# Performance work log

Hardware: AMD Instinct MI355X
Metric: run time of the kernel (lower is better)

Reference implementation:

```python
import jax, jax.numpy as jnp
import numpy as np

S, B, DM, H, DFF = 2048, 4, 1024, 16, 4096
DK = DM // H  # 64, dv == dk
EPS = 1e-5

def layer_norm(x, g, b):
    mu = jnp.mean(x, axis=-1, keepdims=True)
    var = jnp.var(x, axis=-1, keepdims=True)
    return (x - mu) * jax.lax.rsqrt(var + EPS) * g + b

def setup_inputs() -> dict:
    key = jax.random.key(0)
    ks = jax.random.split(key, 12)
    sc = 0.02
    return {
        "X": jax.random.normal(ks[0], (S, B, DM), dtype=jnp.float32),
        # stacked per-head projections: weight [H, dk, dm], bias [H, dk]
        "WQ_w": jax.random.normal(ks[1], (H, DK, DM), dtype=jnp.float32) * sc,
        "WQ_b": jnp.zeros((H, DK), dtype=jnp.float32),
        "WK_w": jax.random.normal(ks[2], (H, DK, DM), dtype=jnp.float32) * sc,
        "WK_b": jnp.zeros((H, DK), dtype=jnp.float32),
        "WV_w": jax.random.normal(ks[3], (H, DK, DM), dtype=jnp.float32) * sc,
        "WV_b": jnp.zeros((H, DK), dtype=jnp.float32),
        "WO_w": jax.random.normal(ks[4], (DM, H * DK), dtype=jnp.float32) * sc,
        "WO_b": jnp.zeros((DM,), dtype=jnp.float32),
        "ln1_g": jnp.ones((DM,), dtype=jnp.float32),
        "ln1_b": jnp.zeros((DM,), dtype=jnp.float32),
        "W1": jax.random.normal(ks[5], (DFF, DM), dtype=jnp.float32) * sc,
        "b1": jnp.zeros((DFF,), dtype=jnp.float32),
        "W2": jax.random.normal(ks[6], (DM, DFF), dtype=jnp.float32) * sc,
        "b2": jnp.zeros((DM,), dtype=jnp.float32),
        "ln2_g": jnp.ones((DM,), dtype=jnp.float32),
        "ln2_b": jnp.zeros((DM,), dtype=jnp.float32),
    }

def reference(X, WQ_w, WQ_b, WK_w, WK_b, WV_w, WV_b, WO_w, WO_b,
              ln1_g, ln1_b, W1, b1, W2, b2, ln2_g, ln2_b):
    # --- self-attention (encoder: no causal mask, no key_mask, drop=0) ---
    # X: [S, B, DM]; per-head Q/K/V: [S, B, H, DK]
    Q = jnp.einsum('sbd,hkd->sbhk', X, WQ_w) + WQ_b
    K = jnp.einsum('sbd,hkd->sbhk', X, WK_w) + WK_b
    V = jnp.einsum('sbd,hvd->sbhv', X, WV_w) + WV_b
    scores = jnp.einsum('sbhk,lbhk->sbhl', Q, K) / jnp.sqrt(jnp.float32(DK))
    attn = jax.nn.softmax(scores, axis=-1)  # softmax over keys l
    ctx = jnp.einsum('sbhl,lbhv->sbhv', attn, V)
    # concat heads (head-major order matches torch.concat over head list)
    ctx = ctx.reshape(S, B, H * DK)
    y = ctx @ WO_w.T + WO_b
    X1 = layer_norm(y + X, ln1_g, ln1_b)
    # --- MLP (1 hidden layer, ReLU) ---
    h = jax.nn.relu(X1 @ W1.T + b1)
    m = h @ W2.T + b2
    return layer_norm(m + X1, ln2_g, ln2_b)
```

## Files before the change

### kernel.cpp

```cpp
#include <hip/hip_runtime.h>
#include <stdint.h>

typedef short bf16x8 __attribute__((ext_vector_type(8)));
typedef float f32x4 __attribute__((ext_vector_type(4)));
typedef float f32x16 __attribute__((ext_vector_type(16)));

__device__ __forceinline__ float bf2f(uint16_t u) {
    union { uint32_t i; float f; } c; c.i = ((uint32_t)u) << 16; return c.f;
}
__device__ __forceinline__ uint16_t f2bf(float f) {
    union { float f; uint32_t i; } c; c.f = f;
    uint32_t x = c.i;
    return (uint16_t)((x + 0x7fffu + ((x >> 16) & 1u)) >> 16);
}
__device__ __forceinline__ uint32_t pack2t(float lo, float hi) {
    union { float f; uint32_t u; } a, b;
    a.f = lo; b.f = hi;
    return __builtin_amdgcn_perm(b.u, a.u, 0x07060302u);
}

__device__ __forceinline__ void load_lds16(const void* g, void* lds) {
    using gp_t = const __attribute__((address_space(1))) uint32_t*;
    using lp_t = __attribute__((address_space(3))) uint32_t*;
    __builtin_amdgcn_global_load_lds(
        reinterpret_cast<gp_t>(reinterpret_cast<uintptr_t>(g)),
        reinterpret_cast<lp_t>((uint32_t)reinterpret_cast<uintptr_t>(lds)),
        16, 0, 0);
}

__global__ __launch_bounds__(256) void cvt_all(
    const float* __restrict__ X,
    const float* __restrict__ wqf, const float* __restrict__ wkf,
    const float* __restrict__ wvf, const float* __restrict__ wof,
    const float* __restrict__ w1f, const float* __restrict__ w2f,
    const float* __restrict__ bqf, const float* __restrict__ bkf,
    const float* __restrict__ bvf, const float* __restrict__ bof,
    const float* __restrict__ b1f, const float* __restrict__ b2f,
    uint16_t* __restrict__ Xb, uint16_t* __restrict__ wd, uint16_t* __restrict__ bd)
{
    const int b = blockIdx.x, tid = threadIdx.x;
    const size_t M = 1048576ull;
    const float* s; uint16_t* d; size_t i, off;
    if (b < 8192) {
        i = ((size_t)b * 256 + tid) * 4;
        s = X; off = i; d = Xb;
    } else if (b < 20480) {
        i = ((size_t)(b - 8192) * 256 + tid) * 4;
        d = wd;
        if (i < M)           { s = wqf; off = i; }
        else if (i < 2 * M)  { s = wkf; off = i - M; }
        else if (i < 3 * M)  { s = wvf; off = i - 2 * M; }
        else if (i < 4 * M)  { s = wof; off = i - 3 * M; }
        else if (i < 8 * M)  { s = w1f; off = i - 4 * M; }
        else                 { s = w2f; off = i - 8 * M; }
    } else {
        int j = tid * 4;
        d = bd;
        for (int p = 0; p < 9; ++p, j += 1024) {
            const float* sb; int ob;
            if (j < 1024)      { sb = bqf; ob = j; }
            else if (j < 2048) { sb = bkf; ob = j - 1024; }
            else if (j < 3072) { sb = bvf; ob = j - 2048; }
            else if (j < 4096) { sb = bof; ob = j - 3072; }
            else if (j < 8192) { sb = b1f; ob = j - 4096; }
            else               { sb = b2f; ob = j - 8192; }
            float4 x = *(const float4*)(sb + ob);
            ushort4 u;
            u.x = f2bf(x.x); u.y = f2bf(x.y); u.z = f2bf(x.z); u.w = f2bf(x.w);
            *(ushort4*)(d + j) = u;
        }
        return;
    }
    float4 x = *(const float4*)(s + off);
    ushort4 u;
    u.x = f2bf(x.x); u.y = f2bf(x.y); u.z = f2bf(x.z); u.w = f2bf(x.w);
    *(ushort4*)(d + i) = u;
}

template<int MODE, int NT>
__global__ __launch_bounds__(256) void gemm_bt(
    const uint16_t* __restrict__ A, const uint16_t* __restrict__ B,
    const uint16_t* __restrict__ bias, uint16_t* __restrict__ C,
    int K, int N, int relu)
{
    const int CT = NT / 32;
    __shared__ uint16_t sA[128 * 64];
    __shared__ uint16_t sB[NT * 64];
    const int tid = threadIdx.x;
    const int w = tid >> 6, ln = tid & 63;
    const int m = ln & 15, q = ln >> 4;
    const int wr = w >> 1, wc = w & 1;
    const int tm = blockIdx.y * 128, tn = blockIdx.x * NT;

    f32x4 zero = {0.f, 0.f, 0.f, 0.f};
    f32x4 acc[4][CT];
#pragma unroll
    for (int i = 0; i < 4; ++i)
#pragma unroll
        for (int j = 0; j < CT; ++j) acc[i][j] = zero;

    const int sr = tid >> 3;
    const int sc_ = tid & 7;
    const int g = sc_ ^ (sr & 7);

    for (int k0 = 0; k0 < K; k0 += 64) {
        __syncthreads();
#pragma unroll
        for (int i = 0; i < 4; ++i) {
            int r = i * 32 + sr;
            load_lds16(A + (size_t)(tm + r) * K + k0 + g * 8, &sA[(i * 32 + w * 8) * 64]);
        }
#pragma unroll
        for (int i = 0; i < NT / 32; ++i) {
            int r = i * 32 + sr;
            load_lds16(B + (size_t)(tn + r) * K + k0 + g * 8, &sB[(i * 32 + w * 8) * 64]);
        }
        __syncthreads();
#pragma unroll
        for (int kk = 0; kk < 2; ++kk) {
            bf16x8 af[4], bfr[CT];
            const int s = (kk * 4 + q) ^ (m & 7);
#pragma unroll
            for (int rt = 0; rt < 4; ++rt) {
                int R = wr * 64 + rt * 16 + m;
                af[rt] = *(const bf16x8*)&sA[R * 64 + s * 8];
            }
#pragma unroll
            for (int ct = 0; ct < CT; ++ct) {
                int R = wc * (NT / 2) + ct * 16 + m;
                bfr[ct] = *(const bf16x8*)&sB[R * 64 + s * 8];
            }
#pragma unroll
            for (int rt = 0; rt < 4; ++rt)
#pragma unroll
                for (int ct = 0; ct < CT; ++ct)
                    acc[rt][ct] = __builtin_amdgcn_mfma_f32_16x16x32_bf16(
                        af[rt], bfr[ct], acc[rt][ct], 0, 0, 0);
        }
    }

    const int sect = tn >> 10;
#pragma unroll
    for (int ct = 0; ct < CT; ++ct) {
        int col = tn + wc * (NT / 2) + ct * 16 + m;
        float bv = bf2f(bias[col]);
#pragma unroll
        for (int rt = 0; rt < 4; ++rt) {
            int rowb = tm + wr * 64 + rt * 16 + q * 4;
#pragma unroll
            for (int rg = 0; rg < 4; ++rg) {
                int t = rowb + rg;
                float v = acc[rt][ct][rg] + bv;
                if (relu) v = fmaxf(v, 0.f);
                size_t off;
                if (MODE == 0) {
                    off = (size_t)t * N + col;
                } else {
                    int c = col & 1023;
                    int bh = (t & 3) * 16 + (c >> 6);
                    if (sect == 0) {
                        off = (size_t)bh * 131072 + (t >> 2) * 64 + (c & 63);
                        v *= 0.18033688f;
                    } else if (sect == 1) {
                        off = 8388608ull + (size_t)bh * 131072 + (t >> 2) * 64 + (c & 63);
                    } else {
                        off = 16777216ull + (size_t)bh * 131072 + (size_t)(c & 63) * 2048 + (t >> 2);
                    }
                }
                C[off] = f2bf(v);
            }
        }
    }
}

__global__ __launch_bounds__(256) void attn2(
    const uint16_t* __restrict__ Qh, const uint16_t* __restrict__ Kh,
    const uint16_t* __restrict__ Vt, uint16_t* __restrict__ CTX)
{
    __shared__ uint16_t sK[64 * 64];
    __shared__ uint16_t sV[64 * 64];
    __shared__ uint16_t sP[128 * 72];

    const int tid = threadIdx.x;
    const int w = tid >> 6, ln = tid & 63;
    const int m5 = ln & 31, h5 = ln >> 5;
    const int bh = blockIdx.x, qt = blockIdx.y;
    const uint16_t* Qb = Qh + (size_t)bh * 131072;
    const uint16_t* Kb = Kh + (size_t)bh * 131072;
    const uint16_t* Vb = Vt + (size_t)bh * 131072;

    const int qrow = qt * 128 + w * 32 + m5;
    bf16x8 qf[4];
#pragma unroll
    for (int ks = 0; ks < 4; ++ks)
        qf[ks] = *(const bf16x8*)(Qb + (size_t)qrow * 64 + ks * 16 + h5 * 8);

    f32x16 Oa[2];
#pragma unroll
    for (int nb = 0; nb < 2; ++nb)
#pragma unroll
        for (int i = 0; i < 16; ++i) Oa[nb][i] = 0.f;
    float psum = 0.f;

    const int sr = tid >> 3;
    const int sc_ = tid & 7;
    const int g = sc_ ^ (sr & 7);

    for (int c = 0; c < 32; ++c) {
        __syncthreads();
        load_lds16(Kb + (size_t)(c * 64 + sr) * 64 + g * 8,        &sK[tid * 8]);
        load_lds16(Kb + (size_t)(c * 64 + sr + 32) * 64 + g * 8,   &sK[2048 + tid * 8]);
        load_lds16(Vb + (size_t)sr * 2048 + c * 64 + g * 8,        &sV[tid * 8]);
        load_lds16(Vb + (size_t)(sr + 32) * 2048 + c * 64 + g * 8, &sV[2048 + tid * 8]);
        __syncthreads();

#pragma unroll
        for (int kb = 0; kb < 2; ++kb) {
            f32x16 acc;
#pragma unroll
            for (int i = 0; i < 16; ++i) acc[i] = 0.f;
#pragma unroll
            for (int ks = 0; ks < 4; ++ks) {
                int row = kb * 32 + m5;
                int ph = (2 * ks + h5) ^ (m5 & 7);
                bf16x8 kf = *(const bf16x8*)&sK[row * 64 + ph * 8];
                acc = __builtin_amdgcn_mfma_f32_32x32x16_bf16(kf, qf[ks], acc, 0, 0, 0);
            }
#pragma unroll
            for (int a = 0; a < 4; ++a) {
                float p0 = exp2f(acc[4 * a + 0]);
                float p1 = exp2f(acc[4 * a + 1]);
                float p2 = exp2f(acc[4 * a + 2]);
                float p3 = exp2f(acc[4 * a + 3]);
                psum += (p0 + p1) + (p2 + p3);
                uint2 d;
                d.x = pack2t(p0, p1);
                d.y = pack2t(p2, p3);
                int log8 = kb * 8 + 2 * a + h5;
                int ph8 = log8 ^ (m5 & 7);
                *(uint2*)&sP[(w * 32 + m5) * 72 + ph8 * 4] = d;
            }
        }

#pragma unroll
        for (int ks = 0; ks < 4; ++ks) {
            int pr = w * 32 + m5;
            int la = 4 * ks + 2 * h5;
            uint2 lo = *(const uint2*)&sP[pr * 72 + ((la) ^ (m5 & 7)) * 4];
            uint2 hi = *(const uint2*)&sP[pr * 72 + ((la + 1) ^ (m5 & 7)) * 4];
            union { uint2 u[2]; bf16x8 v; } pu;
            pu.u[0] = lo; pu.u[1] = hi;
#pragma unroll
            for (int nb = 0; nb < 2; ++nb) {
                int vrow = nb * 32 + m5;
                int ph = (2 * ks + h5) ^ (m5 & 7);
                bf16x8 vf = *(const bf16x8*)&sV[vrow * 64 + ph * 8];
                Oa[nb] = __builtin_amdgcn_mfma_f32_32x32x16_bf16(pu.v, vf, Oa[nb], 0, 0, 0);
            }
        }
    }

    float l = psum + __shfl_xor(psum, 32);
    float linv = 1.f / l;
    float li[16];
#pragma unroll
    for (int a = 0; a < 4; ++a)
#pragma unroll
        for (int r = 0; r < 4; ++r)
            li[4 * a + r] = __shfl(linv, r + 8 * a + 4 * h5);

    const int b_ = bh >> 4, h_ = bh & 15;
#pragma unroll
    for (int nb = 0; nb < 2; ++nb)
#pragma unroll
        for (int a = 0; a < 4; ++a)
#pragma unroll
            for (int r = 0; r < 4; ++r) {
                int qr = r + 8 * a + 4 * h5;
                int s = qt * 128 + w * 32 + qr;
                int col = h_ * 64 + nb * 32 + m5;
                CTX[(size_t)(s * 4 + b_) * 1024 + col] = f2bf(Oa[nb][4 * a + r] * li[4 * a + r]);
            }
}

template<bool RES_F32, bool OUT_F32>
__global__ __launch_bounds__(256) void ln_resid(
    const uint16_t* __restrict__ Y, const void* __restrict__ Xp,
    const float* __restrict__ G, const float* __restrict__ Bv,
    void* __restrict__ Op)
{
    const int row = blockIdx.x, tid = threadIdx.x;
    const size_t base = (size_t)row * 1024 + tid * 4;
    ushort4 yv = *(const ushort4*)(Y + base);
    float x0, x1, x2, x3;
    if (RES_F32) {
        float4 xv = *(const float4*)((const float*)Xp + base);
        x0 = xv.x; x1 = xv.y; x2 = xv.z; x3 = xv.w;
    } else {
        ushort4 xv = *(const ushort4*)((const uint16_t*)Xp + base);
        x0 = bf2f(xv.x); x1 = bf2f(xv.y); x2 = bf2f(xv.z); x3 = bf2f(xv.w);
    }
    float v0 = bf2f(yv.x) + x0;
    float v1 = bf2f(yv.y) + x1;
    float v2 = bf2f(yv.z) + x2;
    float v3 = bf2f(yv.w) + x3;
    float s = v0 + v1 + v2 + v3;
    float ss = v0 * v0 + v1 * v1 + v2 * v2 + v3 * v3;
#pragma unroll
    for (int off = 32; off > 0; off >>= 1) {
        s += __shfl_down(s, off);
        ss += __shfl_down(ss, off);
    }
    __shared__ float rs[4], rss[4];
    if ((tid & 63) == 0) { rs[tid >> 6] = s; rss[tid >> 6] = ss; }
    __syncthreads();
    float S = rs[0] + rs[1] + rs[2] + rs[3];
    float SS = rss[0] + rss[1] + rss[2] + rss[3];
    const float invn = 1.f / 1024.f;
    float mu = S * invn;
    float var = SS * invn - mu * mu;
    float rstd = rsqrtf(var + 1e-5f);
    float4 gv = *(const float4*)(G + tid * 4);
    float4 bv = *(const float4*)(Bv + tid * 4);
    float o0 = (v0 - mu) * rstd * gv.x + bv.x;
    float o1 = (v1 - mu) * rstd * gv.y + bv.y;
    float o2 = (v2 - mu) * rstd * gv.z + bv.z;
    float o3 = (v3 - mu) * rstd * gv.w + bv.w;
    if (OUT_F32) {
        float4 o = {o0, o1, o2, o3};
        *(float4*)((float*)Op + base) = o;
    } else {
        ushort4 o;
        o.x = f2bf(o0); o.y = f2bf(o1); o.z = f2bf(o2); o.w = f2bf(o3);
        *(ushort4*)((uint16_t*)Op + base) = o;
    }
}

extern "C" void kernel_launch(void* const* d_in, const int* in_sizes, int n_in,
                              void* d_out, int out_size, void* d_ws, size_t ws_size,
                              hipStream_t stream)
{
    const float* X    = (const float*)d_in[0];
    const float* WQw  = (const float*)d_in[1];
    const float* WQb  = (const float*)d_in[2];
    const float* WKw  = (const float*)d_in[3];
    const float* WKb  = (const float*)d_in[4];
    const float* WVw  = (const float*)d_in[5];
    const float* WVb  = (const float*)d_in[6];
    const float* WOw  = (const float*)d_in[7];
    const float* WOb  = (const float*)d_in[8];
    const float* ln1g = (const float*)d_in[9];
    const float* ln1b = (const float*)d_in[10];
    const float* W1   = (const float*)d_in[11];
    const float* b1   = (const float*)d_in[12];
    const float* W2   = (const float*)d_in[13];
    const float* b2   = (const float*)d_in[14];
    const float* ln2g = (const float*)d_in[15];
    const float* ln2b = (const float*)d_in[16];

    uint16_t* ws = (uint16_t*)d_ws;
    const size_t E = 8192ull * 1024ull;
    const size_t MW = 1048576ull;
    uint16_t* Xb   = ws;
    uint16_t* qh   = ws + E;
    uint16_t* kh   = ws + 2 * E;
    uint16_t* vt   = ws + 3 * E;
    uint16_t* ctx  = ws + 4 * E;
    uint16_t* y    = qh;
    uint16_t* x1   = kh;
    uint16_t* m2   = vt;
    uint16_t* hbuf = ws + 5 * E;
    uint16_t* wq   = ws + 9 * E;
    uint16_t* wo   = wq + 3 * MW;
    uint16_t* w1   = wo + MW;
    uint16_t* w2   = w1 + 4 * MW;
    uint16_t* bq   = w2 + 4 * MW;
    uint16_t* bo   = bq + 3072;
    uint16_t* bb1  = bo + 1024;
    uint16_t* bb2  = bb1 + 4096;

    cvt_all<<<dim3(20481), dim3(256), 0, stream>>>(
        X, WQw, WKw, WVw, WOw, W1, W2, WQb, WKb, WVb, WOb, b1, b2,
        Xb, wq, bq);

    dim3 blk(256);
    gemm_bt<3, 128><<<dim3(24, 64), blk, 0, stream>>>(Xb,   wq, bq,  qh,   1024, 3072, 0);
    attn2<<<dim3(64, 16), blk, 0, stream>>>(qh, kh, vt, ctx);
    gemm_bt<0, 64><<<dim3(16, 64),  blk, 0, stream>>>(ctx,  wo, bo,  y,    1024, 1024, 0);
    ln_resid<true, false><<<dim3(8192), blk, 0, stream>>>(y, X, ln1g, ln1b, x1);
    gemm_bt<0, 128><<<dim3(32, 64), blk, 0, stream>>>(x1,   w1, bb1, hbuf, 1024, 4096, 1);
    gemm_bt<0, 64><<<dim3(16, 64),  blk, 0, stream>>>(hbuf, w2, bb2, m2,   4096, 1024, 0);
    ln_resid<false, true><<<dim3(8192), blk, 0, stream>>>(m2, x1, ln2g, ln2b, d_out);
}
```

Baseline: 554.6 us.

## Double-buffer K/V tiles and keep softmax probabilities in registers via permlane32 swap

The attention kernel now double-buffers the K and V LDS tiles. The next chunk is prefetched with global_load_lds while the current one is computed, which leaves one barrier per iteration instead of two. The probability tile no longer round-trips through an LDS scratch buffer: the bf16-packed exp values are rearranged into the MFMA A-operand layout with v_permlane32_swap, and exp2f is replaced by the hardware exp2 builtin. This trades extra LDS for the second buffer and relies on the barrier draining the async loads for correctness.

```diff
diff --git a/kernel.cpp b/kernel.cpp
--- a/kernel.cpp
+++ b/kernel.cpp
@@ -17,6 +17,24 @@
     union { float f; uint32_t u; } a, b;
     a.f = lo; b.f = hi;
     return __builtin_amdgcn_perm(b.u, a.u, 0x07060302u);
+}
+
+__device__ __forceinline__ float exp2r(float x) {
+#if __has_builtin(__builtin_amdgcn_exp2f)
+    return __builtin_amdgcn_exp2f(x);
+#else
+    return exp2f(x);
+#endif
+}
+
+__device__ __forceinline__ void plane32_swap(uint32_t& a, uint32_t& b) {
+#if __has_builtin(__builtin_amdgcn_permlane32_swap)
+    typedef unsigned int u32x2 __attribute__((ext_vector_type(2)));
+    u32x2 r = __builtin_amdgcn_permlane32_swap(a, b, false, false);
+    a = r[0]; b = r[1];
+#else
+    asm volatile("v_permlane32_swap_b32 %0, %1" : "+v"(a), "+v"(b));
+#endif
 }
 
 __device__ __forceinline__ void load_lds16(const void* g, void* lds) {
@@ -177,9 +195,8 @@
     const uint16_t* __restrict__ Qh, const uint16_t* __restrict__ Kh,
     const uint16_t* __restrict__ Vt, uint16_t* __restrict__ CTX)
 {
-    __shared__ uint16_t sK[64 * 64];
-    __shared__ uint16_t sV[64 * 64];
-    __shared__ uint16_t sP[128 * 72];
+    __shared__ uint16_t sK[2][64 * 64];
+    __shared__ uint16_t sV[2][64 * 64];
 
     const int tid = threadIdx.x;
     const int w = tid >> 6, ln = tid & 63;
@@ -203,17 +220,29 @@
     float psum = 0.f;
 
     const int sr = tid >> 3;
-    const int sc_ = tid & 7;
-    const int g = sc_ ^ (sr & 7);
+    const int g = (tid & 7) ^ (sr & 7);
+
+    {
+        load_lds16(Kb + (size_t)sr * 64 + g * 8,            &sK[0][tid * 8]);
+        load_lds16(Kb + (size_t)(sr + 32) * 64 + g * 8,     &sK[0][2048 + tid * 8]);
+        load_lds16(Vb + (size_t)sr * 2048 + g * 8,          &sV[0][tid * 8]);
+        load_lds16(Vb + (size_t)(sr + 32) * 2048 + g * 8,   &sV[0][2048 + tid * 8]);
+    }
 
     for (int c = 0; c < 32; ++c) {
+        const int cur = c & 1;
         __syncthreads();
-        load_lds16(Kb + (size_t)(c * 64 + sr) * 64 + g * 8,        &sK[tid * 8]);
-        load_lds16(Kb + (size_t)(c * 64 + sr + 32) * 64 + g * 8,   &sK[2048 + tid * 8]);
-        load_lds16(Vb + (size_t)sr * 2048 + c * 64 + g * 8,        &sV[tid * 8]);
-        load_lds16(Vb + (size_t)(sr + 32) * 2048 + c * 64 + g * 8, &sV[2048 + tid * 8]);
-        __syncthreads();
-
+        if (c + 1 < 32) {
+            const int nc = c + 1;
+            uint16_t* kd = &sK[cur ^ 1][0];
+            uint16_t* vd = &sV[cur ^ 1][0];
+            load_lds16(Kb + (size_t)(nc * 64 + sr) * 64 + g * 8,        kd + tid * 8);
+            load_lds16(Kb + (size_t)(nc * 64 + sr + 32) * 64 + g * 8,   kd + 2048 + tid * 8);
+            load_lds16(Vb + (size_t)sr * 2048 + nc * 64 + g * 8,        vd + tid * 8);
+            load_lds16(Vb + (size_t)(sr + 32) * 2048 + nc * 64 + g * 8, vd + 2048 + tid * 8);
+        }
+
+        bf16x8 pf[4];
 #pragma unroll
         for (int kb = 0; kb < 2; ++kb) {
             f32x16 acc;
@@ -223,39 +252,40 @@
             for (int ks = 0; ks < 4; ++ks) {
                 int row = kb * 32 + m5;
                 int ph = (2 * ks + h5) ^ (m5 & 7);
-                bf16x8 kf = *(const bf16x8*)&sK[row * 64 + ph * 8];
+                bf16x8 kf = *(const bf16x8*)&sK[cur][row * 64 + ph * 8];
                 acc = __builtin_amdgcn_mfma_f32_32x32x16_bf16(kf, qf[ks], acc, 0, 0, 0);
             }
 #pragma unroll
-            for (int a = 0; a < 4; ++a) {
-                float p0 = exp2f(acc[4 * a + 0]);
-                float p1 = exp2f(acc[4 * a + 1]);
-                float p2 = exp2f(acc[4 * a + 2]);
-                float p3 = exp2f(acc[4 * a + 3]);
-                psum += (p0 + p1) + (p2 + p3);
-                uint2 d;
-                d.x = pack2t(p0, p1);
-                d.y = pack2t(p2, p3);
-                int log8 = kb * 8 + 2 * a + h5;
-                int ph8 = log8 ^ (m5 & 7);
-                *(uint2*)&sP[(w * 32 + m5) * 72 + ph8 * 4] = d;
+            for (int ksl = 0; ksl < 2; ++ksl) {
+                float p0 = exp2r(acc[8 * ksl + 0]);
+                float p1 = exp2r(acc[8 * ksl + 1]);
+                float p2 = exp2r(acc[8 * ksl + 2]);
+                float p3 = exp2r(acc[8 * ksl + 3]);
+                float p4 = exp2r(acc[8 * ksl + 4]);
+                float p5 = exp2r(acc[8 * ksl + 5]);
+                float p6 = exp2r(acc[8 * ksl + 6]);
+                float p7 = exp2r(acc[8 * ksl + 7]);
+                psum += ((p0 + p1) + (p2 + p3)) + ((p4 + p5) + (p6 + p7));
+                uint32_t x0 = pack2t(p0, p1);
+                uint32_t x1 = pack2t(p2, p3);
+                uint32_t y0 = pack2t(p4, p5);
+                uint32_t y1 = pack2t(p6, p7);
+                plane32_swap(x0, y0);
+                plane32_swap(x1, y1);
+                union { uint32_t u[4]; bf16x8 v; } pu;
+                pu.u[0] = x0; pu.u[1] = x1; pu.u[2] = y0; pu.u[3] = y1;
+                pf[kb * 2 + ksl] = pu.v;
             }
         }
 
 #pragma unroll
         for (int ks = 0; ks < 4; ++ks) {
-            int pr = w * 32 + m5;
-            int la = 4 * ks + 2 * h5;
-            uint2 lo = *(const uint2*)&sP[pr * 72 + ((la) ^ (m5 & 7)) * 4];
-            uint2 hi = *(const uint2*)&sP[pr * 72 + ((la + 1) ^ (m5 & 7)) * 4];
-            union { uint2 u[2]; bf16x8 v; } pu;
-            pu.u[0] = lo; pu.u[1] = hi;
 #pragma unroll
             for (int nb = 0; nb < 2; ++nb) {
                 int vrow = nb * 32 + m5;
                 int ph = (2 * ks + h5) ^ (m5 & 7);
-                bf16x8 vf = *(const bf16x8*)&sV[vrow * 64 + ph * 8];
-                Oa[nb] = __builtin_amdgcn_mfma_f32_32x32x16_bf16(pu.v, vf, Oa[nb], 0, 0, 0);
+                bf16x8 vf = *(const bf16x8*)&sV[cur][vrow * 64 + ph * 8];
+                Oa[nb] = __builtin_amdgcn_mfma_f32_32x32x16_bf16(pf[ks], vf, Oa[nb], 0, 0, 0);
             }
         }
     }
```

Result: no change. 543.8 us (-1.9%).
